# Kernel tuning notes

Hardware: AMD Instinct MI355X
Metric: run time of the kernel (lower is better)

The kernel has to match this reference:

```python
import jax, jax.numpy as jnp
import numpy as np

NDIM = 3
RADIUS = 0.14
MAX_GRID_DIM = 96
MAX_COLLISIONS = 128
B, N, M, C = 4, 4096, 4096, 16


def setup_inputs() -> dict:
    key = jax.random.key(0)
    k1, k2, k3 = jax.random.split(key, 3)
    locs = jax.random.uniform(k1, (B, N, NDIM), dtype=jnp.float32)
    data = jax.random.normal(k2, (B, N, C), dtype=jnp.float32)
    qlocs = jax.random.uniform(k3, (B, M, NDIM), dtype=jnp.float32)
    return {"locs": locs, "data": data, "qlocs": qlocs}


def _hashgrid_idxs(locs, radius, max_grid_dim):
    """Replicates hashgrid_order: assign each particle a flat grid-cell ID and
    return the permutation (new -> old index) that sorts particles by cell."""
    lower = locs.min(axis=1)                                   # [B,D]
    upper = locs.max(axis=1)                                   # [B,D]
    grid_dims = jnp.ceil(jnp.clip((upper - lower) / radius, 0.0, max_grid_dim))
    center = (lower + upper) * 0.5
    lower = center - grid_dims * radius * 0.5                  # grid lower corner
    cell = jnp.floor((locs - lower[:, None, :]) / radius)
    cell = jnp.clip(cell, 0.0, grid_dims[:, None, :] - 1.0).astype(jnp.int32)
    gd = jnp.maximum(grid_dims.astype(jnp.int32), 1)           # [B,D]
    # row-major strides per batch: stride[d] = prod(gd[d+1:])
    rev = jnp.cumprod(gd[:, ::-1], axis=1)[:, ::-1]            # [B,D]
    strides = jnp.concatenate(
        [rev[:, 1:], jnp.ones((gd.shape[0], 1), jnp.int32)], axis=1)
    cell_ids = (cell * strides[:, None, :]).sum(-1)            # [B,N]
    # stable sort by cell id -> idxs[b, i] = original index of particle now at i
    idxs = jnp.argsort(cell_ids, axis=1)
    return idxs


def reference(locs, data, qlocs):
    idxs = _hashgrid_idxs(locs, RADIUS, MAX_GRID_DIM)
    locs_r = jnp.take_along_axis(locs, idxs[..., None], axis=1)   # [B,N,D]
    data_r = jnp.take_along_axis(data, idxs[..., None], axis=1)   # [B,N,C]

    # Radius search of qlocs against the cell-sorted particles. Neighbor indices
    # are w.r.t. the reordered locs, listed in ascending reordered-index order
    # (cell order), capped at MAX_COLLISIONS, padded with -1.
    qn = (qlocs * qlocs).sum(-1)                                  # [B,M]
    pn = (locs_r * locs_r).sum(-1)                                # [B,N]
    cross = jnp.einsum('bmd,bnd->bmn', qlocs, locs_r)             # [B,M,N]
    dist2 = qn[:, :, None] + pn[:, None, :] - 2.0 * cross         # [B,M,N]
    mask = dist2 <= RADIUS * RADIUS
    # stable argsort of ~mask puts in-radius particles first, in index order
    order = jnp.argsort(~mask, axis=-1)
    neighbors = order[..., :MAX_COLLISIONS].astype(jnp.int32)     # [B,M,K]
    count = mask.sum(-1)                                          # [B,M]
    valid = jnp.arange(MAX_COLLISIONS) < count[..., None]
    neighbors = jnp.where(valid, neighbors, jnp.int32(-1))
    return locs_r, data_r, idxs.astype(jnp.int32), neighbors
```

## Files before the change

### kernel.cpp

```cpp
#include <hip/hip_runtime.h>
#include <stdint.h>

#define BB 4
#define NN 4096
#define MM 4096
#define CC 16
#define KMAX 128

static constexpr int LOCSR_OFF = 0;
static constexpr int DATAR_OFF = BB * NN * 3;
static constexpr int IDXS_OFF  = DATAR_OFF + BB * NN * CC;
static constexpr int NB_OFF    = IDXS_OFF + BB * NN;

static constexpr float RAD_F = 0.14f;
static constexpr float R2F   = (float)(0.14 * 0.14);

static constexpr int MAXC    = 96 * 96 * 96;
static constexpr int CSTRIDE = MAXC + 8;

__global__ void __launch_bounds__(256) k_bbox(const float* __restrict__ locs,
                                              float* __restrict__ pmm) {
    int blk = blockIdx.x;
    int b = blk >> 4, s = blk & 15, t = threadIdx.x;
    int i = s * 256 + t;
    const float* p = locs + (b * NN + i) * 3;
    float x0 = p[0], x1 = p[1], x2 = p[2];
    __shared__ float sm[6][256];
    sm[0][t] = x0; sm[1][t] = x1; sm[2][t] = x2;
    sm[3][t] = x0; sm[4][t] = x1; sm[5][t] = x2;
    __syncthreads();
    for (int st = 128; st > 0; st >>= 1) {
        if (t < st) {
            sm[0][t] = fminf(sm[0][t], sm[0][t + st]);
            sm[1][t] = fminf(sm[1][t], sm[1][t + st]);
            sm[2][t] = fminf(sm[2][t], sm[2][t + st]);
            sm[3][t] = fmaxf(sm[3][t], sm[3][t + st]);
            sm[4][t] = fmaxf(sm[4][t], sm[4][t + st]);
            sm[5][t] = fmaxf(sm[5][t], sm[5][t + st]);
        }
        __syncthreads();
    }
    if (t == 0) {
        float* o = pmm + blk * 6;
        o[0] = sm[0][0]; o[1] = sm[1][0]; o[2] = sm[2][0];
        o[3] = sm[3][0]; o[4] = sm[4][0]; o[5] = sm[5][0];
    }
}

__global__ void __launch_bounds__(1024) k_rank(const float* __restrict__ locs,
                                               const float* __restrict__ data,
                                               const float* __restrict__ pmm,
                                               float* __restrict__ out,
                                               float4* __restrict__ sp4,
                                               unsigned* __restrict__ cs_sorted,
                                               float* __restrict__ gp) {
    __shared__ uint4 keys4[NN / 4];
    __shared__ int partial[16][64];
    __shared__ int s_dst[64];
    __shared__ float sp_low[3], sp_gdf[3];
    __shared__ int sp_s0, sp_s1;
    int blk = blockIdx.x;
    int b = blk >> 6;
    int t = threadIdx.x;
    int wave = t >> 6, lane = t & 63;

    if (t == 0) {
        const float* pm = pmm + b * 96;
        float mn0 = 1e30f, mn1 = 1e30f, mn2 = 1e30f;
        float mx0 = -1e30f, mx1 = -1e30f, mx2 = -1e30f;
#pragma unroll
        for (int k = 0; k < 16; ++k) {
            mn0 = fminf(mn0, pm[k * 6 + 0]);
            mn1 = fminf(mn1, pm[k * 6 + 1]);
            mn2 = fminf(mn2, pm[k * 6 + 2]);
            mx0 = fmaxf(mx0, pm[k * 6 + 3]);
            mx1 = fmaxf(mx1, pm[k * 6 + 4]);
            mx2 = fmaxf(mx2, pm[k * 6 + 5]);
        }
        float lo[3] = {mn0, mn1, mn2}, up[3] = {mx0, mx1, mx2};
        float low2[3], gdf[3];
        int gdi[3];
#pragma unroll
        for (int d = 0; d < 3; ++d) {
            float u = __fdiv_rn(__fsub_rn(up[d], lo[d]), RAD_F);
            u = fminf(fmaxf(u, 0.0f), 96.0f);
            float g = ceilf(u);
            float center = __fmul_rn(__fadd_rn(lo[d], up[d]), 0.5f);
            low2[d] = __fsub_rn(center, __fmul_rn(__fmul_rn(g, RAD_F), 0.5f));
            gdf[d] = g;
            gdi[d] = max((int)g, 1);
        }
        sp_low[0] = low2[0]; sp_low[1] = low2[1]; sp_low[2] = low2[2];
        sp_gdf[0] = gdf[0];  sp_gdf[1] = gdf[1];  sp_gdf[2] = gdf[2];
        sp_s0 = gdi[1] * gdi[2];
        sp_s1 = gdi[2];
        if ((blk & 63) == 0) {
            float* o = gp + b * 12;
            o[0] = low2[0]; o[1] = low2[1]; o[2] = low2[2];
            o[3] = gdf[0];  o[4] = gdf[1];  o[5] = gdf[2];
            ((int*)o)[6]  = gdi[1] * gdi[2];
            ((int*)o)[7]  = gdi[2];
            ((int*)o)[8]  = gdi[0] * gdi[1] * gdi[2];
            ((int*)o)[9]  = gdi[0];
            ((int*)o)[10] = gdi[1];
            ((int*)o)[11] = gdi[2];
        }
    }
    __syncthreads();

    {
        float l0 = sp_low[0], l1 = sp_low[1], l2 = sp_low[2];
        float g0 = sp_gdf[0], g1 = sp_gdf[1], g2 = sp_gdf[2];
        int s0 = sp_s0, s1 = sp_s1;
        const float4* lp = (const float4*)(locs + b * NN * 3) + t * 3;
        float4 A = lp[0], Bv = lp[1], Cv = lp[2];
        float ex[4] = {A.x, A.w, Bv.z, Cv.y};
        float ey[4] = {A.y, Bv.x, Bv.w, Cv.z};
        float ez[4] = {A.z, Bv.y, Cv.x, Cv.w};
        unsigned kk[4];
#pragma unroll
        for (int j = 0; j < 4; ++j) {
            float c0 = fminf(fmaxf(floorf(__fdiv_rn(__fsub_rn(ex[j], l0), RAD_F)), 0.0f), __fsub_rn(g0, 1.0f));
            float c1 = fminf(fmaxf(floorf(__fdiv_rn(__fsub_rn(ey[j], l1), RAD_F)), 0.0f), __fsub_rn(g1, 1.0f));
            float c2 = fminf(fmaxf(floorf(__fdiv_rn(__fsub_rn(ez[j], l2), RAD_F)), 0.0f), __fsub_rn(g2, 1.0f));
            unsigned cell = (unsigned)((int)c0 * s0 + (int)c1 * s1 + (int)c2);
            kk[j] = cell * 4096u + (unsigned)(4 * t + j);
        }
        keys4[t] = make_uint4(kk[0], kk[1], kk[2], kk[3]);
    }
    __syncthreads();

    int i = (blk & 63) * 64 + lane;
    unsigned key = ((const unsigned*)keys4)[i];
    uint4 mv = keys4[wave * 64 + lane];
    int rank = 0;
#pragma unroll
    for (int s = 0; s < 64; ++s) {
        unsigned a  = (unsigned)__builtin_amdgcn_readlane((int)mv.x, s);
        unsigned b2 = (unsigned)__builtin_amdgcn_readlane((int)mv.y, s);
        unsigned c2 = (unsigned)__builtin_amdgcn_readlane((int)mv.z, s);
        unsigned d2 = (unsigned)__builtin_amdgcn_readlane((int)mv.w, s);
        rank += (int)(a < key) + (int)(b2 < key) + (int)(c2 < key) + (int)(d2 < key);
    }
    partial[wave][lane] = rank;
    __syncthreads();
    if (wave == 0) {
        int r = 0;
#pragma unroll
        for (int w = 0; w < 16; ++w) r += partial[w][lane];
        s_dst[lane] = r;
    }
    __syncthreads();
    if (wave == 0) {
        int src = b * NN + i;
        int dst = b * NN + s_dst[lane];
        float x = locs[src * 3 + 0], y = locs[src * 3 + 1], z = locs[src * 3 + 2];
        out[IDXS_OFF + dst] = (float)i;
        out[LOCSR_OFF + dst * 3 + 0] = x;
        out[LOCSR_OFF + dst * 3 + 1] = y;
        out[LOCSR_OFF + dst * 3 + 2] = z;
        cs_sorted[dst] = key;
        float pn = __fadd_rn(__fadd_rn(__fmul_rn(x, x), __fmul_rn(y, y)), __fmul_rn(z, z));
        sp4[dst] = make_float4(x, y, z, pn);
    } else if (wave <= 4) {
        int p = lane;
        int ii = (blk & 63) * 64 + p;
        int dst = b * NN + s_dst[p];
        int c = wave - 1;
        const float4* dsrc = (const float4*)(data + (b * NN + ii) * 16);
        float4* ddst = (float4*)(out + DATAR_OFF + dst * 16);
        ddst[c] = dsrc[c];
    }
}

__global__ void __launch_bounds__(256) k_cellstart(const unsigned* __restrict__ cs_sorted,
                                                   const float* __restrict__ gp,
                                                   int* __restrict__ cell_start) {
    int b = blockIdx.y;
    int nc = ((const int*)(gp + b * 12))[8];
    const unsigned* cs = cs_sorted + b * NN;
    int* cst = cell_start + b * CSTRIDE;
    for (int c = blockIdx.x * 256 + threadIdx.x; c <= nc; c += gridDim.x * 256) {
        int lo = 0, hi = NN;
        while (lo < hi) {
            int mid = (lo + hi) >> 1;
            if ((int)(cs[mid] >> 12) < c) lo = mid + 1; else hi = mid;
        }
        cst[c] = lo;
    }
}

__device__ inline void axis_range(float qd, float lo, int gd, int* c0, int* c1) {
    const float DL = RAD_F + 1e-4f;
    float vlo = (qd - DL - lo) / RAD_F;
    float vhi = (qd + DL - lo) / RAD_F;
    int a = (int)floorf(vlo), b = (int)floorf(vhi);
    *c0 = min(max(a, 0), gd - 1);
    *c1 = min(max(b, 0), gd - 1);
}

__global__ void __launch_bounds__(256, 6) k_neighbors(const float* __restrict__ qlocs,
                                                      const float4* __restrict__ sp4,
                                                      const int* __restrict__ cell_start,
                                                      const float* __restrict__ gp,
                                                      float* __restrict__ out) {
    int blk = blockIdx.x;
    int b = blk >> 10;
    int wave = threadIdx.x >> 6, lane = threadIdx.x & 63;
    int m = (blk & 1023) * 4 + wave;
    const float* o = gp + b * 12;
    const int* oi = (const int*)o;
    int s0 = oi[6], s1 = oi[7];
    int gd0 = oi[9], gd1 = oi[10], gd2 = oi[11];
    const float* q = qlocs + (b * MM + m) * 3;
    float q0 = q[0], q1 = q[1], q2 = q[2];
    float qn = __fadd_rn(__fadd_rn(__fmul_rn(q0, q0), __fmul_rn(q1, q1)), __fmul_rn(q2, q2));
    int cx0, cx1, cy0, cy1, cz0, cz1;
    axis_range(q0, o[0], gd0, &cx0, &cx1);
    axis_range(q1, o[1], gd1, &cy0, &cy1);
    axis_range(q2, o[2], gd2, &cz0, &cz1);
    const float4* sp = sp4 + b * NN;
    const int* cst = cell_start + b * CSTRIDE;
    float* nb = out + NB_OFF + (b * MM + m) * KMAX;

    int ps_[9], pe_[9];
#pragma unroll
    for (int dx = 0; dx < 3; ++dx) {
#pragma unroll
        for (int dy = 0; dy < 3; ++dy) {
            int k = dx * 3 + dy;
            int cx = cx0 + dx, cy = cy0 + dy;
            bool v = (cx <= cx1) && (cy <= cy1);
            int base = cx * s0 + cy * s1;
            int i0 = v ? base + cz0 : 0;
            int i1 = v ? base + cz1 + 1 : 0;
            int a = cst[i0];
            int e = cst[i1];
            ps_[k] = v ? a : 0;
            pe_[k] = v ? e : 0;
        }
    }
    int pre_[10];
    pre_[0] = 0;
#pragma unroll
    for (int k = 0; k < 9; ++k) pre_[k + 1] = pre_[k] + max(pe_[k] - ps_[k], 0);
    int T = pre_[9];

    int count = 0;
    for (int l0 = 0; l0 < T; l0 += 64) {
        int l = l0 + lane;
        int p = 0;
#pragma unroll
        for (int k = 0; k < 9; ++k) {
            bool in = (l >= pre_[k]) && (l < pre_[k + 1]);
            p = in ? (ps_[k] + (l - pre_[k])) : p;
        }
        float4 P = sp[p];
        float cross = fmaf(q2, P.z, fmaf(q1, P.y, __fmul_rn(q0, P.x)));
        float dist2 = __fsub_rn(__fadd_rn(qn, P.w), __fmul_rn(2.0f, cross));
        bool hit = (l < T) && (dist2 <= R2F);
        unsigned long long bal = __ballot(hit);
        if (hit) {
            int pos = count + __popcll(bal & ((1ull << lane) - 1ull));
            if (pos < KMAX) nb[pos] = (float)p;
        }
        count += __popcll(bal);
        if (count >= KMAX) break;
    }
    for (int j = count + lane; j < KMAX; j += 64) nb[j] = -1.0f;
}

extern "C" void kernel_launch(void* const* d_in, const int* in_sizes, int n_in,
                              void* d_out, int out_size, void* d_ws, size_t ws_size,
                              hipStream_t stream) {
    const float* locs  = (const float*)d_in[0];
    const float* data  = (const float*)d_in[1];
    const float* qlocs = (const float*)d_in[2];
    float* out = (float*)d_out;
    char* ws = (char*)d_ws;
    float*    gp        = (float*)ws;
    float*    pmm       = (float*)(ws + 512);
    unsigned* cs_sorted = (unsigned*)(ws + 4608);
    float4*   sp4       = (float4*)(ws + 4608 + 65536);
    int* cell_start = (int*)(ws + 4608 + 65536 + BB * NN * sizeof(float4));

    k_bbox<<<BB * 16, 256, 0, stream>>>(locs, pmm);
    k_rank<<<BB * 64, 1024, 0, stream>>>(locs, data, pmm, out, sp4, cs_sorted, gp);
    k_cellstart<<<dim3(32, BB), 256, 0, stream>>>(cs_sorted, gp, cell_start);
    k_neighbors<<<BB * 1024, 256, 0, stream>>>(qlocs, sp4, cell_start, gp, out);
}
```

Baseline: 93.72 us.

## Fuse all four stages into one cooperative kernel with grid syncs

Combines the bbox reduction, ranking/scatter, cell-start binary search and neighbor search into a single cooperative kernel. The stages are separated by grid-wide barriers instead of separate launches. The bbox reduction now uses wave shuffles over 64-element slices, and grid parameters stay in shared memory instead of a global buffer. This removes three launch gaps and the global parameter round trip. In exchange the neighbor stage runs on only 256 blocks of 1024 threads with each wave handling 4 queries sequentially, which lowers parallelism and latency hiding compared with the earlier 4096-block launch.

New measurement: 180.7 us. +92.9%, slower.

```diff
diff --git a/kernel.cpp b/kernel.cpp
--- a/kernel.cpp
+++ b/kernel.cpp
@@ -1,5 +1,8 @@
 #include <hip/hip_runtime.h>
+#include <hip/hip_cooperative_groups.h>
 #include <stdint.h>
+
+namespace cg = cooperative_groups;
 
 #define BB 4
 #define NN 4096
@@ -18,58 +21,64 @@
 static constexpr int MAXC    = 96 * 96 * 96;
 static constexpr int CSTRIDE = MAXC + 8;
 
-__global__ void __launch_bounds__(256) k_bbox(const float* __restrict__ locs,
-                                              float* __restrict__ pmm) {
-    int blk = blockIdx.x;
-    int b = blk >> 4, s = blk & 15, t = threadIdx.x;
-    int i = s * 256 + t;
-    const float* p = locs + (b * NN + i) * 3;
-    float x0 = p[0], x1 = p[1], x2 = p[2];
-    __shared__ float sm[6][256];
-    sm[0][t] = x0; sm[1][t] = x1; sm[2][t] = x2;
-    sm[3][t] = x0; sm[4][t] = x1; sm[5][t] = x2;
-    __syncthreads();
-    for (int st = 128; st > 0; st >>= 1) {
-        if (t < st) {
-            sm[0][t] = fminf(sm[0][t], sm[0][t + st]);
-            sm[1][t] = fminf(sm[1][t], sm[1][t + st]);
-            sm[2][t] = fminf(sm[2][t], sm[2][t + st]);
-            sm[3][t] = fmaxf(sm[3][t], sm[3][t + st]);
-            sm[4][t] = fmaxf(sm[4][t], sm[4][t + st]);
-            sm[5][t] = fmaxf(sm[5][t], sm[5][t + st]);
-        }
-        __syncthreads();
-    }
-    if (t == 0) {
-        float* o = pmm + blk * 6;
-        o[0] = sm[0][0]; o[1] = sm[1][0]; o[2] = sm[2][0];
-        o[3] = sm[3][0]; o[4] = sm[4][0]; o[5] = sm[5][0];
-    }
+__device__ inline void axis_range(float qd, float lo, int gd, int* c0, int* c1) {
+    const float DL = RAD_F + 1e-4f;
+    float vlo = (qd - DL - lo) / RAD_F;
+    float vhi = (qd + DL - lo) / RAD_F;
+    int a = (int)floorf(vlo), b = (int)floorf(vhi);
+    *c0 = min(max(a, 0), gd - 1);
+    *c1 = min(max(b, 0), gd - 1);
 }
 
-__global__ void __launch_bounds__(1024) k_rank(const float* __restrict__ locs,
-                                               const float* __restrict__ data,
-                                               const float* __restrict__ pmm,
-                                               float* __restrict__ out,
-                                               float4* __restrict__ sp4,
-                                               unsigned* __restrict__ cs_sorted,
-                                               float* __restrict__ gp) {
+__global__ void __launch_bounds__(1024, 4)
+k_mega(const float* __restrict__ locs,
+       const float* __restrict__ data,
+       const float* __restrict__ qlocs,
+       float* __restrict__ out,
+       float* __restrict__ pmm,
+       unsigned* __restrict__ cs_sorted,
+       float4* __restrict__ sp4,
+       int* __restrict__ cell_start) {
+    cg::grid_group grid = cg::this_grid();
     __shared__ uint4 keys4[NN / 4];
     __shared__ int partial[16][64];
     __shared__ int s_dst[64];
     __shared__ float sp_low[3], sp_gdf[3];
-    __shared__ int sp_s0, sp_s1;
+    __shared__ int sp_gdi[3], sp_s0, sp_s1, sp_nc;
+
     int blk = blockIdx.x;
     int b = blk >> 6;
     int t = threadIdx.x;
     int wave = t >> 6, lane = t & 63;
 
+    if (wave == 0) {
+        int slice = blk & 63;
+        const float* p = locs + (b * NN + slice * 64 + lane) * 3;
+        float mn0 = p[0], mn1 = p[1], mn2 = p[2];
+        float mx0 = mn0, mx1 = mn1, mx2 = mn2;
+#pragma unroll
+        for (int off = 32; off > 0; off >>= 1) {
+            mn0 = fminf(mn0, __shfl_xor(mn0, off));
+            mn1 = fminf(mn1, __shfl_xor(mn1, off));
+            mn2 = fminf(mn2, __shfl_xor(mn2, off));
+            mx0 = fmaxf(mx0, __shfl_xor(mx0, off));
+            mx1 = fmaxf(mx1, __shfl_xor(mx1, off));
+            mx2 = fmaxf(mx2, __shfl_xor(mx2, off));
+        }
+        if (lane == 0) {
+            float* o = pmm + blk * 6;
+            o[0] = mn0; o[1] = mn1; o[2] = mn2;
+            o[3] = mx0; o[4] = mx1; o[5] = mx2;
+        }
+    }
+    grid.sync();
+
     if (t == 0) {
-        const float* pm = pmm + b * 96;
+        const float* pm = pmm + b * 64 * 6;
         float mn0 = 1e30f, mn1 = 1e30f, mn2 = 1e30f;
         float mx0 = -1e30f, mx1 = -1e30f, mx2 = -1e30f;
 #pragma unroll
-        for (int k = 0; k < 16; ++k) {
+        for (int k = 0; k < 64; ++k) {
             mn0 = fminf(mn0, pm[k * 6 + 0]);
             mn1 = fminf(mn1, pm[k * 6 + 1]);
             mn2 = fminf(mn2, pm[k * 6 + 2]);
@@ -78,33 +87,19 @@
             mx2 = fmaxf(mx2, pm[k * 6 + 5]);
         }
         float lo[3] = {mn0, mn1, mn2}, up[3] = {mx0, mx1, mx2};
-        float low2[3], gdf[3];
-        int gdi[3];
 #pragma unroll
         for (int d = 0; d < 3; ++d) {
             float u = __fdiv_rn(__fsub_rn(up[d], lo[d]), RAD_F);
             u = fminf(fmaxf(u, 0.0f), 96.0f);
             float g = ceilf(u);
             float center = __fmul_rn(__fadd_rn(lo[d], up[d]), 0.5f);
-            low2[d] = __fsub_rn(center, __fmul_rn(__fmul_rn(g, RAD_F), 0.5f));
-            gdf[d] = g;
-            gdi[d] = max((int)g, 1);
-        }
-        sp_low[0] = low2[0]; sp_low[1] = low2[1]; sp_low[2] = low2[2];
-        sp_gdf[0] = gdf[0];  sp_gdf[1] = gdf[1];  sp_gdf[2] = gdf[2];
-        sp_s0 = gdi[1] * gdi[2];
-        sp_s1 = gdi[2];
-        if ((blk & 63) == 0) {
-            float* o = gp + b * 12;
-            o[0] = low2[0]; o[1] = low2[1]; o[2] = low2[2];
-            o[3] = gdf[0];  o[4] = gdf[1];  o[5] = gdf[2];
-            ((int*)o)[6]  = gdi[1] * gdi[2];
-            ((int*)o)[7]  = gdi[2];
-            ((int*)o)[8]  = gdi[0] * gdi[1] * gdi[2];
-            ((int*)o)[9]  = gdi[0];
-            ((int*)o)[10] = gdi[1];
-            ((int*)o)[11] = gdi[2];
-        }
+            sp_low[d] = __fsub_rn(center, __fmul_rn(__fmul_rn(g, RAD_F), 0.5f));
+            sp_gdf[d] = g;
+            sp_gdi[d] = max((int)g, 1);
+        }
+        sp_s0 = sp_gdi[1] * sp_gdi[2];
+        sp_s1 = sp_gdi[2];
+        sp_nc = sp_gdi[0] * sp_gdi[1] * sp_gdi[2];
     }
     __syncthreads();
 
@@ -171,103 +166,88 @@
         float4* ddst = (float4*)(out + DATAR_OFF + dst * 16);
         ddst[c] = dsrc[c];
     }
-}
-
-__global__ void __launch_bounds__(256) k_cellstart(const unsigned* __restrict__ cs_sorted,
-                                                   const float* __restrict__ gp,
-                                                   int* __restrict__ cell_start) {
-    int b = blockIdx.y;
-    int nc = ((const int*)(gp + b * 12))[8];
-    const unsigned* cs = cs_sorted + b * NN;
-    int* cst = cell_start + b * CSTRIDE;
-    for (int c = blockIdx.x * 256 + threadIdx.x; c <= nc; c += gridDim.x * 256) {
-        int lo = 0, hi = NN;
-        while (lo < hi) {
-            int mid = (lo + hi) >> 1;
-            if ((int)(cs[mid] >> 12) < c) lo = mid + 1; else hi = mid;
-        }
-        cst[c] = lo;
-    }
-}
-
-__device__ inline void axis_range(float qd, float lo, int gd, int* c0, int* c1) {
-    const float DL = RAD_F + 1e-4f;
-    float vlo = (qd - DL - lo) / RAD_F;
-    float vhi = (qd + DL - lo) / RAD_F;
-    int a = (int)floorf(vlo), b = (int)floorf(vhi);
-    *c0 = min(max(a, 0), gd - 1);
-    *c1 = min(max(b, 0), gd - 1);
-}
-
-__global__ void __launch_bounds__(256, 6) k_neighbors(const float* __restrict__ qlocs,
-                                                      const float4* __restrict__ sp4,
-                                                      const int* __restrict__ cell_start,
-                                                      const float* __restrict__ gp,
-                                                      float* __restrict__ out) {
-    int blk = blockIdx.x;
-    int b = blk >> 10;
-    int wave = threadIdx.x >> 6, lane = threadIdx.x & 63;
-    int m = (blk & 1023) * 4 + wave;
-    const float* o = gp + b * 12;
-    const int* oi = (const int*)o;
-    int s0 = oi[6], s1 = oi[7];
-    int gd0 = oi[9], gd1 = oi[10], gd2 = oi[11];
-    const float* q = qlocs + (b * MM + m) * 3;
-    float q0 = q[0], q1 = q[1], q2 = q[2];
-    float qn = __fadd_rn(__fadd_rn(__fmul_rn(q0, q0), __fmul_rn(q1, q1)), __fmul_rn(q2, q2));
-    int cx0, cx1, cy0, cy1, cz0, cz1;
-    axis_range(q0, o[0], gd0, &cx0, &cx1);
-    axis_range(q1, o[1], gd1, &cy0, &cy1);
-    axis_range(q2, o[2], gd2, &cz0, &cz1);
-    const float4* sp = sp4 + b * NN;
-    const int* cst = cell_start + b * CSTRIDE;
-    float* nb = out + NB_OFF + (b * MM + m) * KMAX;
-
-    int ps_[9], pe_[9];
-#pragma unroll
-    for (int dx = 0; dx < 3; ++dx) {
-#pragma unroll
-        for (int dy = 0; dy < 3; ++dy) {
-            int k = dx * 3 + dy;
-            int cx = cx0 + dx, cy = cy0 + dy;
-            bool v = (cx <= cx1) && (cy <= cy1);
-            int base = cx * s0 + cy * s1;
-            int i0 = v ? base + cz0 : 0;
-            int i1 = v ? base + cz1 + 1 : 0;
-            int a = cst[i0];
-            int e = cst[i1];
-            ps_[k] = v ? a : 0;
-            pe_[k] = v ? e : 0;
-        }
-    }
-    int pre_[10];
-    pre_[0] = 0;
-#pragma unroll
-    for (int k = 0; k < 9; ++k) pre_[k + 1] = pre_[k] + max(pe_[k] - ps_[k], 0);
-    int T = pre_[9];
-
-    int count = 0;
-    for (int l0 = 0; l0 < T; l0 += 64) {
-        int l = l0 + lane;
-        int p = 0;
-#pragma unroll
-        for (int k = 0; k < 9; ++k) {
-            bool in = (l >= pre_[k]) && (l < pre_[k + 1]);
-            p = in ? (ps_[k] + (l - pre_[k])) : p;
-        }
-        float4 P = sp[p];
-        float cross = fmaf(q2, P.z, fmaf(q1, P.y, __fmul_rn(q0, P.x)));
-        float dist2 = __fsub_rn(__fadd_rn(qn, P.w), __fmul_rn(2.0f, cross));
-        bool hit = (l < T) && (dist2 <= R2F);
-        unsigned long long bal = __ballot(hit);
-        if (hit) {
-            int pos = count + __popcll(bal & ((1ull << lane) - 1ull));
-            if (pos < KMAX) nb[pos] = (float)p;
-        }
-        count += __popcll(bal);
-        if (count >= KMAX) break;
-    }
-    for (int j = count + lane; j < KMAX; j += 64) nb[j] = -1.0f;
+    grid.sync();
+
+    {
+        int nc = sp_nc;
+        const unsigned* cs = cs_sorted + b * NN;
+        int* cst = cell_start + b * CSTRIDE;
+        for (int c = (blk & 63) * 1024 + t; c <= nc; c += 64 * 1024) {
+            int lo = 0, hi = NN;
+            while (lo < hi) {
+                int mid = (lo + hi) >> 1;
+                if ((int)(cs[mid] >> 12) < c) lo = mid + 1; else hi = mid;
+            }
+            cst[c] = lo;
+        }
+    }
+    grid.sync();
+
+    {
+        int s0 = sp_s0, s1 = sp_s1;
+        int gd0 = sp_gdi[0], gd1 = sp_gdi[1], gd2 = sp_gdi[2];
+        float lo0 = sp_low[0], lo1 = sp_low[1], lo2 = sp_low[2];
+        const float4* sp = sp4 + b * NN;
+        const int* cst = cell_start + b * CSTRIDE;
+#pragma unroll 1
+        for (int j = 0; j < 4; ++j) {
+            int m = (blk & 63) * 64 + wave * 4 + j;
+            const float* q = qlocs + (b * MM + m) * 3;
+            float q0 = q[0], q1 = q[1], q2 = q[2];
+            float qn = __fadd_rn(__fadd_rn(__fmul_rn(q0, q0), __fmul_rn(q1, q1)), __fmul_rn(q2, q2));
+            int cx0, cx1, cy0, cy1, cz0, cz1;
+            axis_range(q0, lo0, gd0, &cx0, &cx1);
+            axis_range(q1, lo1, gd1, &cy0, &cy1);
+            axis_range(q2, lo2, gd2, &cz0, &cz1);
+            float* nb = out + NB_OFF + (b * MM + m) * KMAX;
+
+            int ps_[9], pe_[9];
+#pragma unroll
+            for (int dx = 0; dx < 3; ++dx) {
+#pragma unroll
+                for (int dy = 0; dy < 3; ++dy) {
+                    int k = dx * 3 + dy;
+                    int cx = cx0 + dx, cy = cy0 + dy;
+                    bool v = (cx <= cx1) && (cy <= cy1);
+                    int base = cx * s0 + cy * s1;
+                    int i0 = v ? base + cz0 : 0;
+                    int i1 = v ? base + cz1 + 1 : 0;
+                    int a = cst[i0];
+                    int e = cst[i1];
+                    ps_[k] = v ? a : 0;
+                    pe_[k] = v ? e : 0;
+                }
+            }
+            int pre_[10];
+            pre_[0] = 0;
+#pragma unroll
+            for (int k = 0; k < 9; ++k) pre_[k + 1] = pre_[k] + max(pe_[k] - ps_[k], 0);
+            int T = pre_[9];
+
+            int count = 0;
+            for (int l0i = 0; l0i < T; l0i += 64) {
+                int l = l0i + lane;
+                int p = 0;
+#pragma unroll
+                for (int k = 0; k < 9; ++k) {
+                    bool in = (l >= pre_[k]) && (l < pre_[k + 1]);
+                    p = in ? (ps_[k] + (l - pre_[k])) : p;
+                }
+                float4 P = sp[p];
+                float cross = fmaf(q2, P.z, fmaf(q1, P.y, __fmul_rn(q0, P.x)));
+                float dist2 = __fsub_rn(__fadd_rn(qn, P.w), __fmul_rn(2.0f, cross));
+                bool hit = (l < T) && (dist2 <= R2F);
+                unsigned long long bal = __ballot(hit);
+                if (hit) {
+                    int pos = count + __popcll(bal & ((1ull << lane) - 1ull));
+                    if (pos < KMAX) nb[pos] = (float)p;
+                }
+                count += __popcll(bal);
+                if (count >= KMAX) break;
+            }
+            for (int jj = count + lane; jj < KMAX; jj += 64) nb[jj] = -1.0f;
+        }
+    }
 }
 
 extern "C" void kernel_launch(void* const* d_in, const int* in_sizes, int n_in,
@@ -278,14 +258,13 @@
     const float* qlocs = (const float*)d_in[2];
     float* out = (float*)d_out;
     char* ws = (char*)d_ws;
-    float*    gp        = (float*)ws;
-    float*    pmm       = (float*)(ws + 512);
-    unsigned* cs_sorted = (unsigned*)(ws + 4608);
-    float4*   sp4       = (float4*)(ws + 4608 + 65536);
-    int* cell_start = (int*)(ws + 4608 + 65536 + BB * NN * sizeof(float4));
-
-    k_bbox<<<BB * 16, 256, 0, stream>>>(locs, pmm);
-    k_rank<<<BB * 64, 1024, 0, stream>>>(locs, data, pmm, out, sp4, cs_sorted, gp);
-    k_cellstart<<<dim3(32, BB), 256, 0, stream>>>(cs_sorted, gp, cell_start);
-    k_neighbors<<<BB * 1024, 256, 0, stream>>>(qlocs, sp4, cell_start, gp, out);
+    float*    pmm       = (float*)ws;
+    unsigned* cs_sorted = (unsigned*)(ws + 8192);
+    float4*   sp4       = (float4*)(ws + 8192 + 65536);
+    int* cell_start = (int*)(ws + 8192 + 65536 + BB * NN * sizeof(float4));
+
+    void* args[] = {(void*)&locs, (void*)&data, (void*)&qlocs, (void*)&out,
+                    (void*)&pmm, (void*)&cs_sorted, (void*)&sp4, (void*)&cell_start};
+    hipLaunchCooperativeKernel(reinterpret_cast<void*>(k_mega),
+                               dim3(256), dim3(1024), args, 0, stream);
 }
```

## Fuse cell-start lookup into neighbor kernel via shared-memory binary search

Applied to the files above, without the earlier changes.

Removes the separate k_cellstart kernel, which binary-searched every grid cell (up to 96^3) into a global cell_start table. Each neighbor block instead loads the batch's 4096 sorted keys (16 KB) into LDS, and lanes of each wave binary-search only the 18 cell-range boundaries that wave needs. This drops a kernel launch and the large cell_start table writes. In exchange, every block reloads the keys into LDS, adds a barrier and 12 search steps per wave, and the larger LDS use may limit occupancy.

Result: faster. 91.48 us (-2.4%).

```diff
diff --git a/kernel.cpp b/kernel.cpp
--- a/kernel.cpp
+++ b/kernel.cpp
@@ -14,9 +14,6 @@
 
 static constexpr float RAD_F = 0.14f;
 static constexpr float R2F   = (float)(0.14 * 0.14);
-
-static constexpr int MAXC    = 96 * 96 * 96;
-static constexpr int CSTRIDE = MAXC + 8;
 
 __global__ void __launch_bounds__(256) k_bbox(const float* __restrict__ locs,
                                               float* __restrict__ pmm) {
@@ -173,23 +170,6 @@
     }
 }
 
-__global__ void __launch_bounds__(256) k_cellstart(const unsigned* __restrict__ cs_sorted,
-                                                   const float* __restrict__ gp,
-                                                   int* __restrict__ cell_start) {
-    int b = blockIdx.y;
-    int nc = ((const int*)(gp + b * 12))[8];
-    const unsigned* cs = cs_sorted + b * NN;
-    int* cst = cell_start + b * CSTRIDE;
-    for (int c = blockIdx.x * 256 + threadIdx.x; c <= nc; c += gridDim.x * 256) {
-        int lo = 0, hi = NN;
-        while (lo < hi) {
-            int mid = (lo + hi) >> 1;
-            if ((int)(cs[mid] >> 12) < c) lo = mid + 1; else hi = mid;
-        }
-        cst[c] = lo;
-    }
-}
-
 __device__ inline void axis_range(float qd, float lo, int gd, int* c0, int* c1) {
     const float DL = RAD_F + 1e-4f;
     float vlo = (qd - DL - lo) / RAD_F;
@@ -201,12 +181,23 @@
 
 __global__ void __launch_bounds__(256, 6) k_neighbors(const float* __restrict__ qlocs,
                                                       const float4* __restrict__ sp4,
-                                                      const int* __restrict__ cell_start,
+                                                      const unsigned* __restrict__ cs_sorted,
                                                       const float* __restrict__ gp,
                                                       float* __restrict__ out) {
+    __shared__ uint4 skeys4[NN / 4];
+    const unsigned* skeys = (const unsigned*)skeys4;
+
     int blk = blockIdx.x;
     int b = blk >> 10;
-    int wave = threadIdx.x >> 6, lane = threadIdx.x & 63;
+    int t = threadIdx.x;
+    int wave = t >> 6, lane = t & 63;
+
+    {
+        const uint4* g = (const uint4*)(cs_sorted + b * NN);
+#pragma unroll
+        for (int j = 0; j < 4; ++j) skeys4[t + 256 * j] = g[t + 256 * j];
+    }
+
     int m = (blk & 1023) * 4 + wave;
     const float* o = gp + b * 12;
     const int* oi = (const int*)o;
@@ -220,10 +211,10 @@
     axis_range(q1, o[1], gd1, &cy0, &cy1);
     axis_range(q2, o[2], gd2, &cz0, &cz1);
     const float4* sp = sp4 + b * NN;
-    const int* cst = cell_start + b * CSTRIDE;
     float* nb = out + NB_OFF + (b * MM + m) * KMAX;
 
-    int ps_[9], pe_[9];
+    unsigned t0_[9], t1_[9];
+    bool va_[9];
 #pragma unroll
     for (int dx = 0; dx < 3; ++dx) {
 #pragma unroll
@@ -232,13 +223,37 @@
             int cx = cx0 + dx, cy = cy0 + dy;
             bool v = (cx <= cx1) && (cy <= cy1);
             int base = cx * s0 + cy * s1;
-            int i0 = v ? base + cz0 : 0;
-            int i1 = v ? base + cz1 + 1 : 0;
-            int a = cst[i0];
-            int e = cst[i1];
-            ps_[k] = v ? a : 0;
-            pe_[k] = v ? e : 0;
-        }
+            va_[k] = v;
+            t0_[k] = v ? (unsigned)(base + cz0) * 4096u : 0u;
+            t1_[k] = v ? (unsigned)(base + cz1 + 1) * 4096u : 0u;
+        }
+    }
+    __syncthreads();
+
+    unsigned tgt = 0u;
+#pragma unroll
+    for (int k = 0; k < 9; ++k) {
+        tgt = (lane == k)      ? t0_[k] : tgt;
+        tgt = (lane == 16 + k) ? t1_[k] : tgt;
+    }
+    int lo = 0, hi = NN;
+#pragma unroll
+    for (int it = 0; it < 12; ++it) {
+        int mid = (lo + hi) >> 1;
+        unsigned v = skeys[mid];
+        bool c = v < tgt;
+        lo = c ? mid + 1 : lo;
+        hi = c ? hi : mid;
+    }
+    int res = lo;
+
+    int ps_[9], pe_[9];
+#pragma unroll
+    for (int k = 0; k < 9; ++k) {
+        int a = __shfl(res, k);
+        int e = __shfl(res, 16 + k);
+        ps_[k] = va_[k] ? a : 0;
+        pe_[k] = va_[k] ? e : 0;
     }
     int pre_[10];
     pre_[0] = 0;
@@ -247,8 +262,8 @@
     int T = pre_[9];
 
     int count = 0;
-    for (int l0 = 0; l0 < T; l0 += 64) {
-        int l = l0 + lane;
+    for (int l0i = 0; l0i < T; l0i += 64) {
+        int l = l0i + lane;
         int p = 0;
 #pragma unroll
         for (int k = 0; k < 9; ++k) {
@@ -282,10 +297,8 @@
     float*    pmm       = (float*)(ws + 512);
     unsigned* cs_sorted = (unsigned*)(ws + 4608);
     float4*   sp4       = (float4*)(ws + 4608 + 65536);
-    int* cell_start = (int*)(ws + 4608 + 65536 + BB * NN * sizeof(float4));
 
     k_bbox<<<BB * 16, 256, 0, stream>>>(locs, pmm);
     k_rank<<<BB * 64, 1024, 0, stream>>>(locs, data, pmm, out, sp4, cs_sorted, gp);
-    k_cellstart<<<dim3(32, BB), 256, 0, stream>>>(cs_sorted, gp, cell_start);
-    k_neighbors<<<BB * 1024, 256, 0, stream>>>(qlocs, sp4, cell_start, gp, out);
-}
+    k_neighbors<<<BB * 1024, 256, 0, stream>>>(qlocs, sp4, cs_sorted, gp, out);
+}
```
